# Performance work log

Hardware: AMD Instinct MI355X
Metric: run time of the kernel (lower is better)

## Reference

```python
import jax, jax.numpy as jnp
import numpy as np

EMBED_DIM = 1024
NUM_HEADS = 16
SCALE = (EMBED_DIM // NUM_HEADS) ** -0.5  # 0.125


def setup_inputs() -> dict:
    key = jax.random.key(0)
    ks = jax.random.split(key, 9)
    B, S, E = 4, 2048, EMBED_DIM
    std = E ** -0.5
    x = jax.random.normal(ks[0], (B, S, E), dtype=jnp.float32)
    Wq = jax.random.normal(ks[1], (E, E), dtype=jnp.float32) * std
    bq = jax.random.normal(ks[2], (E,), dtype=jnp.float32) * 0.01
    Wk = jax.random.normal(ks[3], (E, E), dtype=jnp.float32) * std
    bk = jax.random.normal(ks[4], (E,), dtype=jnp.float32) * 0.01
    Wv = jax.random.normal(ks[5], (E, E), dtype=jnp.float32) * std
    bv = jax.random.normal(ks[6], (E,), dtype=jnp.float32) * 0.01
    Wo = jax.random.normal(ks[7], (E, E), dtype=jnp.float32) * std
    bo = jax.random.normal(ks[8], (E,), dtype=jnp.float32) * 0.01
    return {"x": x, "Wq": Wq, "bq": bq, "Wk": Wk, "bk": bk,
            "Wv": Wv, "bv": bv, "Wo": Wo, "bo": bo}


def reference(x, Wq, bq, Wk, bk, Wv, bv, Wo, bo):
    # torch nn.Linear: y = x @ W.T + b
    q = jnp.einsum('bse,fe->bsf', x, Wq) + bq   # [B,S,E]
    k = jnp.einsum('bse,fe->bsf', x, Wk) + bk
    v = jnp.einsum('bse,fe->bsf', x, Wv) + bv
    # Bilinear (no softmax) attention: scores = (Q K^T) * scale
    scores = jnp.einsum('bse,bte->bst', q, k) * SCALE  # [B,S,S]
    out = jnp.einsum('bst,bte->bse', scores, v)        # [B,S,E]
    return jnp.einsum('bse,fe->bsf', out, Wo) + bo
```

## Files before the change

### kernel.cpp

```cpp
#include <hip/hip_runtime.h>
#include <stdint.h>

typedef __bf16 bf16_t;
typedef __bf16 bf16x8 __attribute__((ext_vector_type(8)));
typedef __bf16 bf16x4 __attribute__((ext_vector_type(4)));
typedef float floatx4 __attribute__((ext_vector_type(4)));

__device__ __forceinline__ void async_copy16(const bf16_t* g, bf16_t* l) {
  __builtin_amdgcn_global_load_lds(
      (const __attribute__((address_space(1))) void*)g,
      (__attribute__((address_space(3))) void*)l, 16, 0, 0);
}

struct CvtSeg { const float* s; bf16_t* d; long n; };
struct CvtArgs { CvtSeg seg[5]; };

__global__ void cvt_multi(CvtArgs a) {
  CvtSeg sg = a.seg[blockIdx.y];
#pragma unroll
  for (int it = 0; it < 4; it++) {
    long i = (((long)blockIdx.x + (long)it * 2048) * 256 + threadIdx.x) * 4;
    if (i < sg.n) {
      float4 f = *(const float4*)(sg.s + i);
      bf16x4 o;
      o[0] = (bf16_t)f.x; o[1] = (bf16_t)f.y; o[2] = (bf16_t)f.z; o[3] = (bf16_t)f.w;
      *(bf16x4*)(sg.d + i) = o;
    }
  }
}

__global__ __launch_bounds__(256, 2) void qkv3(
    const bf16_t* __restrict__ xb,
    const bf16_t* __restrict__ Wq, const bf16_t* __restrict__ Wk, const bf16_t* __restrict__ Wv,
    const float* __restrict__ bq, const float* __restrict__ bk, const float* __restrict__ bv,
    bf16_t* __restrict__ qout, bf16_t* __restrict__ kT, bf16_t* __restrict__ vT) {
  __shared__ bf16_t As[2 * 4096];
  __shared__ bf16_t Bsh[3][2 * 4096];
  const int L = blockIdx.x;
  const int V = (L & 7) * 64 + (L >> 3);
  const int batch = V >> 7;
  const int rr_   = V & 127;
  const int n0 = (rr_ & 7) * 128;
  const int m0 = (rr_ >> 3) * 128;

  const int tid = threadIdx.x, lane = tid & 63, w = tid >> 6;
  const int wr = w >> 1, wc = w & 1, quad = lane >> 4, lm = lane & 15;
  const int ar = lane >> 2;
  const int ak = (((lane & 3) ^ ((ar >> 1) & 3))) * 8;
  const int swz = (lm >> 1) & 3;

  const bf16_t* ag0 = xb + (long)batch * (2048L * 1024) + (long)(m0 + w * 16 + ar) * 1024 + ak;
  const bf16_t* ag1 = ag0 + 64L * 1024;
  const bf16_t* Wp[3] = {Wq, Wk, Wv};
  const bf16_t* bg0[3];
  const bf16_t* bg1[3];
#pragma unroll
  for (int p = 0; p < 3; p++) {
    bg0[p] = Wp[p] + (long)(n0 + w * 16 + ar) * 1024 + ak;
    bg1[p] = bg0[p] + 64L * 1024;
  }

  floatx4 acc[3][4][4];
#pragma unroll
  for (int p = 0; p < 3; p++)
#pragma unroll
    for (int r = 0; r < 4; r++)
#pragma unroll
      for (int c = 0; c < 4; c++)
        acc[p][r][c] = (floatx4){0.f, 0.f, 0.f, 0.f};

  {
    bf16_t* la = As + w * 512;
    async_copy16(ag0, la);
    async_copy16(ag1, la + 2048);
#pragma unroll
    for (int p = 0; p < 3; p++) {
      bf16_t* lb = Bsh[p] + w * 512;
      async_copy16(bg0[p], lb);
      async_copy16(bg1[p], lb + 2048);
    }
  }
  for (int i = 0; i < 32; i++) {
    __syncthreads();
    if (i + 1 < 32) {
      const int buf = (i + 1) & 1, k0 = (i + 1) * 32;
      bf16_t* la = As + buf * 4096 + w * 512;
      async_copy16(ag0 + k0, la);
      async_copy16(ag1 + k0, la + 2048);
#pragma unroll
      for (int p = 0; p < 3; p++) {
        bf16_t* lb = Bsh[p] + buf * 4096 + w * 512;
        async_copy16(bg0[p] + k0, lb);
        async_copy16(bg1[p] + k0, lb + 2048);
      }
    }
    const bf16_t* Ar = As + (i & 1) * 4096;
    bf16x8 afr[4];
#pragma unroll
    for (int r = 0; r < 4; r++)
      afr[r] = *(const bf16x8*)&Ar[(wr * 64 + r * 16 + lm) * 32 + (quad ^ swz) * 8];
#pragma unroll
    for (int p = 0; p < 3; p++) {
      const bf16_t* Br = Bsh[p] + (i & 1) * 4096;
      bf16x8 bfr[4];
#pragma unroll
      for (int c = 0; c < 4; c++)
        bfr[c] = *(const bf16x8*)&Br[(wc * 64 + c * 16 + lm) * 32 + (quad ^ swz) * 8];
#pragma unroll
      for (int r = 0; r < 4; r++)
#pragma unroll
        for (int c = 0; c < 4; c++)
          acc[p][r][c] = __builtin_amdgcn_mfma_f32_16x16x32_bf16(afr[r], bfr[c], acc[p][r][c], 0, 0, 0);
    }
  }

  const int rowBase = m0 + wr * 64, colBase = n0 + wc * 64;
  {
    bf16_t* C = qout + (long)batch * (2048L * 1024);
#pragma unroll
    for (int r = 0; r < 4; r++) {
      const int row = rowBase + r * 16 + quad * 4;
#pragma unroll
      for (int c = 0; c < 4; c++) {
        const int col = colBase + c * 16 + lm;
        const float bv_ = bq[col];
#pragma unroll
        for (int i = 0; i < 4; i++)
          C[(long)(row + i) * 1024 + col] = (bf16_t)(acc[0][r][c][i] + bv_);
      }
    }
  }
#pragma unroll
  for (int p = 1; p < 3; p++) {
    bf16_t* C = ((p == 1) ? kT : vT) + (long)batch * (1024L * 2048);
    const float* bias = (p == 1) ? bk : bv;
#pragma unroll
    for (int r = 0; r < 4; r++) {
      const int row = rowBase + r * 16 + quad * 4;
#pragma unroll
      for (int c = 0; c < 4; c++) {
        const int col = colBase + c * 16 + lm;
        const float bv_ = bias[col];
        bf16x4 pk;
#pragma unroll
        for (int i = 0; i < 4; i++) pk[i] = (bf16_t)(acc[p][r][c][i] + bv_);
        *(bf16x4*)(C + (long)col * 2048 + row) = pk;
      }
    }
  }
}

template<int OUT_MODE, bool HAS_BIAS, int TOTAL, int BPZ>
__global__ __launch_bounds__(256) void gemm_nt64(
    const bf16_t* __restrict__ A, const bf16_t* __restrict__ B,
    void* __restrict__ C, const float* __restrict__ bias,
    int lda, int ldb, int nk, long sA, long sB, long sC, int ldc, float alpha) {
  __shared__ bf16_t As[2 * 4096];
  __shared__ bf16_t Bs[2 * 2048];
  const int L = blockIdx.x;
  const int V = (L & 7) * (TOTAL / 8) + (L >> 3);
  const int batch = V / BPZ;
  const int r_ = V % BPZ;
  const int n0 = (r_ & 15) * 64;
  const int m0 = (r_ >> 4) * 128;

  const int tid = threadIdx.x, lane = tid & 63, w = tid >> 6;
  const int wr = w >> 1, wc = w & 1, quad = lane >> 4, lm = lane & 15;
  const int ar = lane >> 2;
  const int ak = (((lane & 3) ^ ((ar >> 1) & 3))) * 8;
  const int swz = (lm >> 1) & 3;

  const bf16_t* Ab = A + (long)batch * sA;
  const bf16_t* Bb = B + (long)batch * sB;
  const bf16_t* ag0 = Ab + (long)(m0 + w * 16 + ar) * lda + ak;
  const bf16_t* ag1 = ag0 + (long)64 * lda;
  const bf16_t* bg0 = Bb + (long)(n0 + w * 16 + ar) * ldb + ak;

  floatx4 acc[4][2];
#pragma unroll
  for (int r = 0; r < 4; r++)
#pragma unroll
    for (int c = 0; c < 2; c++) acc[r][c] = (floatx4){0.f, 0.f, 0.f, 0.f};

  {
    async_copy16(ag0, As + w * 512);
    async_copy16(ag1, As + w * 512 + 2048);
    async_copy16(bg0, Bs + w * 512);
  }
  for (int i = 0; i < nk; i++) {
    __syncthreads();
    if (i + 1 < nk) {
      const int buf = (i + 1) & 1, k0 = (i + 1) * 32;
      async_copy16(ag0 + k0, As + buf * 4096 + w * 512);
      async_copy16(ag1 + k0, As + buf * 4096 + w * 512 + 2048);
      async_copy16(bg0 + k0, Bs + buf * 2048 + w * 512);
    }
    const bf16_t* Ar = As + (i & 1) * 4096;
    const bf16_t* Br = Bs + (i & 1) * 2048;
    bf16x8 afr[4], bfr[2];
#pragma unroll
    for (int r = 0; r < 4; r++)
      afr[r] = *(const bf16x8*)&Ar[(wr * 64 + r * 16 + lm) * 32 + (quad ^ swz) * 8];
#pragma unroll
    for (int c = 0; c < 2; c++)
      bfr[c] = *(const bf16x8*)&Br[(wc * 32 + c * 16 + lm) * 32 + (quad ^ swz) * 8];
#pragma unroll
    for (int r = 0; r < 4; r++)
#pragma unroll
      for (int c = 0; c < 2; c++)
        acc[r][c] = __builtin_amdgcn_mfma_f32_16x16x32_bf16(afr[r], bfr[c], acc[r][c], 0, 0, 0);
  }

  const int rowBase = m0 + wr * 64, colBase = n0 + wc * 32;
  if (OUT_MODE == 0) {
    bf16_t* Cb = (bf16_t*)C + (long)batch * sC;
#pragma unroll
    for (int r = 0; r < 4; r++) {
      const int row = rowBase + r * 16 + quad * 4;
#pragma unroll
      for (int c = 0; c < 2; c++) {
        const int col = colBase + c * 16 + lm;
        const float bv_ = HAS_BIAS ? bias[col] : 0.f;
#pragma unroll
        for (int i = 0; i < 4; i++)
          Cb[(long)(row + i) * ldc + col] = (bf16_t)(acc[r][c][i] * alpha + bv_);
      }
    }
  } else {
    float* Cf = (float*)C + (long)batch * sC;
#pragma unroll
    for (int r = 0; r < 4; r++) {
      const int row = rowBase + r * 16 + quad * 4;
#pragma unroll
      for (int c = 0; c < 2; c++) {
        const int col = colBase + c * 16 + lm;
        const float bv_ = HAS_BIAS ? bias[col] : 0.f;
#pragma unroll
        for (int i = 0; i < 4; i++)
          Cf[(long)(row + i) * ldc + col] = acc[r][c][i] * alpha + bv_;
      }
    }
  }
}

extern "C" void kernel_launch(void* const* d_in, const int* in_sizes, int n_in,
                              void* d_out, int out_size, void* d_ws, size_t ws_size,
                              hipStream_t stream) {
  const float* x  = (const float*)d_in[0];
  const float* Wq = (const float*)d_in[1];
  const float* bq = (const float*)d_in[2];
  const float* Wk = (const float*)d_in[3];
  const float* bk = (const float*)d_in[4];
  const float* Wv = (const float*)d_in[5];
  const float* bv = (const float*)d_in[6];
  const float* Wo = (const float*)d_in[7];
  const float* bo = (const float*)d_in[8];
  float* out = (float*)d_out;

  const long NX = 8192L * 1024;
  const long NW = 1024L * 1024;
  const long NM = 4L * 1024 * 1024;

  bf16_t* ws  = (bf16_t*)d_ws;
  bf16_t* xb  = ws;
  bf16_t* Wqb = xb + NX;
  bf16_t* Wkb = Wqb + NW;
  bf16_t* Wvb = Wkb + NW;
  bf16_t* Wob = Wvb + NW;
  bf16_t* qb  = Wob + NW;
  bf16_t* kT  = qb + NX;
  bf16_t* vT  = kT + NX;
  bf16_t* MtTb = vT + NX;
  bf16_t* Gb   = xb;

  CvtArgs ca;
  ca.seg[0] = {x,  xb,  NX};
  ca.seg[1] = {Wq, Wqb, NW};
  ca.seg[2] = {Wk, Wkb, NW};
  ca.seg[3] = {Wv, Wvb, NW};
  ca.seg[4] = {Wo, Wob, NW};
  cvt_multi<<<dim3(2048, 5), 256, 0, stream>>>(ca);

  qkv3<<<dim3(512), 256, 0, stream>>>(xb, Wqb, Wkb, Wvb, bq, bk, bv, qb, kT, vT);

  gemm_nt64<0, false, 512, 128><<<dim3(512), 256, 0, stream>>>(
      kT, vT, MtTb, nullptr, 2048, 2048, 64,
      1024L * 2048, 1024L * 2048, 1024L * 1024, 1024, 0.125f);

  gemm_nt64<0, false, 512, 128><<<dim3(512), 256, 0, stream>>>(
      Wob, MtTb, Gb, nullptr, 1024, 1024, 32,
      0L, 1024L * 1024, 1024L * 1024, 1024, 1.0f);

  gemm_nt64<2, true, 1024, 256><<<dim3(1024), 256, 0, stream>>>(
      qb, Gb, out, bo, 1024, 1024, 32,
      2048L * 1024, 1024L * 1024, 2048L * 1024, 1024, 1.0f);
}
```

Baseline: 237.3 us.

## Use 128x128 tiles, split-K for K^T V, and reorder output GEMMs

```diff
diff --git a/kernel.cpp b/kernel.cpp
--- a/kernel.cpp
+++ b/kernel.cpp
@@ -27,6 +27,20 @@
       *(bf16x4*)(sg.d + i) = o;
     }
   }
+}
+
+__global__ void cvt_mhalf(const bf16_t* __restrict__ mh, bf16_t* __restrict__ mt) {
+  const long i = ((long)blockIdx.x * 256 + threadIdx.x) * 8;
+  const long b = i >> 20;
+  const long r = i & ((1L << 20) - 1);
+  const bf16_t* h0 = mh + ((b * 2) << 20) + r;
+  const bf16_t* h1 = h0 + (1L << 20);
+  bf16x8 x0 = *(const bf16x8*)h0;
+  bf16x8 x1 = *(const bf16x8*)h1;
+  bf16x8 o;
+#pragma unroll
+  for (int j = 0; j < 8; j++) o[j] = (bf16_t)((float)x0[j] + (float)x1[j]);
+  *(bf16x8*)(mt + i) = o;
 }
 
 __global__ __launch_bounds__(256, 2) void qkv3(
@@ -150,19 +164,21 @@
   }
 }
 
-template<int OUT_MODE, bool HAS_BIAS, int TOTAL, int BPZ>
-__global__ __launch_bounds__(256) void gemm_nt64(
+template<int OUT_MODE, bool HAS_BIAS, int TOTAL, int BPZ, int KSPLIT>
+__global__ __launch_bounds__(256) void gemm_nt128(
     const bf16_t* __restrict__ A, const bf16_t* __restrict__ B,
     void* __restrict__ C, const float* __restrict__ bias,
     int lda, int ldb, int nk, long sA, long sB, long sC, int ldc, float alpha) {
   __shared__ bf16_t As[2 * 4096];
-  __shared__ bf16_t Bs[2 * 2048];
+  __shared__ bf16_t Bs[2 * 4096];
   const int L = blockIdx.x;
   const int V = (L & 7) * (TOTAL / 8) + (L >> 3);
-  const int batch = V / BPZ;
+  const int zz = V / BPZ;
   const int r_ = V % BPZ;
-  const int n0 = (r_ & 15) * 64;
-  const int m0 = (r_ >> 4) * 128;
+  const int batch = zz / KSPLIT;
+  const long koff = (long)(zz % KSPLIT) * ((long)nk * 32);
+  const int n0 = (r_ & 7) * 128;
+  const int m0 = (r_ >> 3) * 128;
 
   const int tid = threadIdx.x, lane = tid & 63, w = tid >> 6;
   const int wr = w >> 1, wc = w & 1, quad = lane >> 4, lm = lane & 15;
@@ -170,22 +186,24 @@
   const int ak = (((lane & 3) ^ ((ar >> 1) & 3))) * 8;
   const int swz = (lm >> 1) & 3;
 
-  const bf16_t* Ab = A + (long)batch * sA;
-  const bf16_t* Bb = B + (long)batch * sB;
+  const bf16_t* Ab = A + (long)batch * sA + koff;
+  const bf16_t* Bb = B + (long)batch * sB + koff;
   const bf16_t* ag0 = Ab + (long)(m0 + w * 16 + ar) * lda + ak;
   const bf16_t* ag1 = ag0 + (long)64 * lda;
   const bf16_t* bg0 = Bb + (long)(n0 + w * 16 + ar) * ldb + ak;
-
-  floatx4 acc[4][2];
+  const bf16_t* bg1 = bg0 + (long)64 * ldb;
+
+  floatx4 acc[4][4];
 #pragma unroll
   for (int r = 0; r < 4; r++)
 #pragma unroll
-    for (int c = 0; c < 2; c++) acc[r][c] = (floatx4){0.f, 0.f, 0.f, 0.f};
+    for (int c = 0; c < 4; c++) acc[r][c] = (floatx4){0.f, 0.f, 0.f, 0.f};
 
   {
     async_copy16(ag0, As + w * 512);
     async_copy16(ag1, As + w * 512 + 2048);
     async_copy16(bg0, Bs + w * 512);
+    async_copy16(bg1, Bs + w * 512 + 2048);
   }
   for (int i = 0; i < nk; i++) {
     __syncthreads();
@@ -193,32 +211,33 @@
       const int buf = (i + 1) & 1, k0 = (i + 1) * 32;
       async_copy16(ag0 + k0, As + buf * 4096 + w * 512);
       async_copy16(ag1 + k0, As + buf * 4096 + w * 512 + 2048);
-      async_copy16(bg0 + k0, Bs + buf * 2048 + w * 512);
+      async_copy16(bg0 + k0, Bs + buf * 4096 + w * 512);
+      async_copy16(bg1 + k0, Bs + buf * 4096 + w * 512 + 2048);
     }
     const bf16_t* Ar = As + (i & 1) * 4096;
-    const bf16_t* Br = Bs + (i & 1) * 2048;
-    bf16x8 afr[4], bfr[2];
+    const bf16_t* Br = Bs + (i & 1) * 4096;
+    bf16x8 afr[4], bfr[4];
 #pragma unroll
     for (int r = 0; r < 4; r++)
       afr[r] = *(const bf16x8*)&Ar[(wr * 64 + r * 16 + lm) * 32 + (quad ^ swz) * 8];
 #pragma unroll
-    for (int c = 0; c < 2; c++)
-      bfr[c] = *(const bf16x8*)&Br[(wc * 32 + c * 16 + lm) * 32 + (quad ^ swz) * 8];
+    for (int c = 0; c < 4; c++)
+      bfr[c] = *(const bf16x8*)&Br[(wc * 64 + c * 16 + lm) * 32 + (quad ^ swz) * 8];
 #pragma unroll
     for (int r = 0; r < 4; r++)
 #pragma unroll
-      for (int c = 0; c < 2; c++)
+      for (int c = 0; c < 4; c++)
         acc[r][c] = __builtin_amdgcn_mfma_f32_16x16x32_bf16(afr[r], bfr[c], acc[r][c], 0, 0, 0);
   }
 
-  const int rowBase = m0 + wr * 64, colBase = n0 + wc * 32;
+  const int rowBase = m0 + wr * 64, colBase = n0 + wc * 64;
   if (OUT_MODE == 0) {
-    bf16_t* Cb = (bf16_t*)C + (long)batch * sC;
+    bf16_t* Cb = (bf16_t*)C + (long)zz * sC;
 #pragma unroll
     for (int r = 0; r < 4; r++) {
       const int row = rowBase + r * 16 + quad * 4;
 #pragma unroll
-      for (int c = 0; c < 2; c++) {
+      for (int c = 0; c < 4; c++) {
         const int col = colBase + c * 16 + lm;
         const float bv_ = HAS_BIAS ? bias[col] : 0.f;
 #pragma unroll
@@ -227,12 +246,12 @@
       }
     }
   } else {
-    float* Cf = (float*)C + (long)batch * sC;
+    float* Cf = (float*)C + (long)zz * sC;
 #pragma unroll
     for (int r = 0; r < 4; r++) {
       const int row = rowBase + r * 16 + quad * 4;
 #pragma unroll
-      for (int c = 0; c < 2; c++) {
+      for (int c = 0; c < 4; c++) {
         const int col = colBase + c * 16 + lm;
         const float bv_ = HAS_BIAS ? bias[col] : 0.f;
 #pragma unroll
@@ -259,7 +278,6 @@
 
   const long NX = 8192L * 1024;
   const long NW = 1024L * 1024;
-  const long NM = 4L * 1024 * 1024;
 
   bf16_t* ws  = (bf16_t*)d_ws;
   bf16_t* xb  = ws;
@@ -270,8 +288,9 @@
   bf16_t* qb  = Wob + NW;
   bf16_t* kT  = qb + NX;
   bf16_t* vT  = kT + NX;
-  bf16_t* MtTb = vT + NX;
-  bf16_t* Gb   = xb;
+  bf16_t* Mh  = xb;
+  bf16_t* Mtb = kT;
+  bf16_t* Pb  = vT;
 
   CvtArgs ca;
   ca.seg[0] = {x,  xb,  NX};
@@ -283,15 +302,17 @@
 
   qkv3<<<dim3(512), 256, 0, stream>>>(xb, Wqb, Wkb, Wvb, bq, bk, bv, qb, kT, vT);
 
-  gemm_nt64<0, false, 512, 128><<<dim3(512), 256, 0, stream>>>(
-      kT, vT, MtTb, nullptr, 2048, 2048, 64,
+  gemm_nt128<0, false, 512, 64, 2><<<dim3(512), 256, 0, stream>>>(
+      vT, kT, Mh, nullptr, 2048, 2048, 32,
       1024L * 2048, 1024L * 2048, 1024L * 1024, 1024, 0.125f);
 
-  gemm_nt64<0, false, 512, 128><<<dim3(512), 256, 0, stream>>>(
-      Wob, MtTb, Gb, nullptr, 1024, 1024, 32,
-      0L, 1024L * 1024, 1024L * 1024, 1024, 1.0f);
-
-  gemm_nt64<2, true, 1024, 256><<<dim3(1024), 256, 0, stream>>>(
-      qb, Gb, out, bo, 1024, 1024, 32,
+  cvt_mhalf<<<dim3(2048), 256, 0, stream>>>(Mh, Mtb);
+
+  gemm_nt128<0, false, 512, 128, 1><<<dim3(512), 256, 0, stream>>>(
+      qb, Mtb, Pb, nullptr, 1024, 1024, 32,
       2048L * 1024, 1024L * 1024, 2048L * 1024, 1024, 1.0f);
-}
+
+  gemm_nt128<2, true, 512, 128, 1><<<dim3(512), 256, 0, stream>>>(
+      Pb, Wob, out, bo, 1024, 1024, 32,
+      2048L * 1024, 0L, 2048L * 1024, 1024, 1.0f);
+}
```

Result: no change. 239.5 us (+0.9%).

## Use per-warp private LDS staging with 128x128 tiles in GEMMs

Applied to the files above, without the earlier changes.

```diff
diff --git a/kernel.cpp b/kernel.cpp
--- a/kernel.cpp
+++ b/kernel.cpp
@@ -151,18 +151,17 @@
 }
 
 template<int OUT_MODE, bool HAS_BIAS, int TOTAL, int BPZ>
-__global__ __launch_bounds__(256) void gemm_nt64(
+__global__ __launch_bounds__(256) void gemm_wp(
     const bf16_t* __restrict__ A, const bf16_t* __restrict__ B,
     void* __restrict__ C, const float* __restrict__ bias,
     int lda, int ldb, int nk, long sA, long sB, long sC, int ldc, float alpha) {
-  __shared__ bf16_t As[2 * 4096];
-  __shared__ bf16_t Bs[2 * 2048];
+  __shared__ bf16_t Ls[4 * 8192];
   const int L = blockIdx.x;
   const int V = (L & 7) * (TOTAL / 8) + (L >> 3);
   const int batch = V / BPZ;
   const int r_ = V % BPZ;
-  const int n0 = (r_ & 15) * 64;
-  const int m0 = (r_ >> 4) * 128;
+  const int n0 = (r_ & 7) * 128;
+  const int m0 = (r_ >> 3) * 128;
 
   const int tid = threadIdx.x, lane = tid & 63, w = tid >> 6;
   const int wr = w >> 1, wc = w & 1, quad = lane >> 4, lm = lane & 15;
@@ -170,55 +169,61 @@
   const int ak = (((lane & 3) ^ ((ar >> 1) & 3))) * 8;
   const int swz = (lm >> 1) & 3;
 
+  bf16_t* Lw = Ls + w * 8192;
   const bf16_t* Ab = A + (long)batch * sA;
   const bf16_t* Bb = B + (long)batch * sB;
-  const bf16_t* ag0 = Ab + (long)(m0 + w * 16 + ar) * lda + ak;
-  const bf16_t* ag1 = ag0 + (long)64 * lda;
-  const bf16_t* bg0 = Bb + (long)(n0 + w * 16 + ar) * ldb + ak;
-
-  floatx4 acc[4][2];
+  const bf16_t* agA = Ab + (long)(m0 + wr * 64 + ar) * lda + ak;
+  const bf16_t* agB = Bb + (long)(n0 + wc * 64 + ar) * ldb + ak;
+
+  auto STAGE = [&](int t, int b) {
+    const int k0 = t * 32;
+    bf16_t* d = Lw + b * 4096;
+#pragma unroll
+    for (int j = 0; j < 4; j++)
+      async_copy16(agA + (long)j * 16 * lda + k0, d + j * 512);
+#pragma unroll
+    for (int j = 0; j < 4; j++)
+      async_copy16(agB + (long)j * 16 * ldb + k0, d + 2048 + j * 512);
+  };
+
+  floatx4 acc[4][4];
 #pragma unroll
   for (int r = 0; r < 4; r++)
 #pragma unroll
-    for (int c = 0; c < 2; c++) acc[r][c] = (floatx4){0.f, 0.f, 0.f, 0.f};
-
-  {
-    async_copy16(ag0, As + w * 512);
-    async_copy16(ag1, As + w * 512 + 2048);
-    async_copy16(bg0, Bs + w * 512);
-  }
+    for (int c = 0; c < 4; c++) acc[r][c] = (floatx4){0.f, 0.f, 0.f, 0.f};
+
+  STAGE(0, 0);
   for (int i = 0; i < nk; i++) {
-    __syncthreads();
     if (i + 1 < nk) {
-      const int buf = (i + 1) & 1, k0 = (i + 1) * 32;
-      async_copy16(ag0 + k0, As + buf * 4096 + w * 512);
-      async_copy16(ag1 + k0, As + buf * 4096 + w * 512 + 2048);
-      async_copy16(bg0 + k0, Bs + buf * 2048 + w * 512);
-    }
-    const bf16_t* Ar = As + (i & 1) * 4096;
-    const bf16_t* Br = Bs + (i & 1) * 2048;
-    bf16x8 afr[4], bfr[2];
+      STAGE(i + 1, (i + 1) & 1);
+      asm volatile("s_waitcnt vmcnt(8)" ::: "memory");
+    } else {
+      asm volatile("s_waitcnt vmcnt(0)" ::: "memory");
+    }
+    const bf16_t* Aw = Lw + (i & 1) * 4096;
+    const bf16_t* Bw = Aw + 2048;
+    bf16x8 afr[4], bfr[4];
 #pragma unroll
     for (int r = 0; r < 4; r++)
-      afr[r] = *(const bf16x8*)&Ar[(wr * 64 + r * 16 + lm) * 32 + (quad ^ swz) * 8];
-#pragma unroll
-    for (int c = 0; c < 2; c++)
-      bfr[c] = *(const bf16x8*)&Br[(wc * 32 + c * 16 + lm) * 32 + (quad ^ swz) * 8];
+      afr[r] = *(const bf16x8*)&Aw[(r * 16 + lm) * 32 + (quad ^ swz) * 8];
+#pragma unroll
+    for (int c = 0; c < 4; c++)
+      bfr[c] = *(const bf16x8*)&Bw[(c * 16 + lm) * 32 + (quad ^ swz) * 8];
 #pragma unroll
     for (int r = 0; r < 4; r++)
 #pragma unroll
-      for (int c = 0; c < 2; c++)
+      for (int c = 0; c < 4; c++)
         acc[r][c] = __builtin_amdgcn_mfma_f32_16x16x32_bf16(afr[r], bfr[c], acc[r][c], 0, 0, 0);
   }
 
-  const int rowBase = m0 + wr * 64, colBase = n0 + wc * 32;
+  const int rowBase = m0 + wr * 64, colBase = n0 + wc * 64;
   if (OUT_MODE == 0) {
     bf16_t* Cb = (bf16_t*)C + (long)batch * sC;
 #pragma unroll
     for (int r = 0; r < 4; r++) {
       const int row = rowBase + r * 16 + quad * 4;
 #pragma unroll
-      for (int c = 0; c < 2; c++) {
+      for (int c = 0; c < 4; c++) {
         const int col = colBase + c * 16 + lm;
         const float bv_ = HAS_BIAS ? bias[col] : 0.f;
 #pragma unroll
@@ -232,7 +237,7 @@
     for (int r = 0; r < 4; r++) {
       const int row = rowBase + r * 16 + quad * 4;
 #pragma unroll
-      for (int c = 0; c < 2; c++) {
+      for (int c = 0; c < 4; c++) {
         const int col = colBase + c * 16 + lm;
         const float bv_ = HAS_BIAS ? bias[col] : 0.f;
 #pragma unroll
@@ -259,7 +264,6 @@
 
   const long NX = 8192L * 1024;
   const long NW = 1024L * 1024;
-  const long NM = 4L * 1024 * 1024;
 
   bf16_t* ws  = (bf16_t*)d_ws;
   bf16_t* xb  = ws;
@@ -270,8 +274,8 @@
   bf16_t* qb  = Wob + NW;
   bf16_t* kT  = qb + NX;
   bf16_t* vT  = kT + NX;
-  bf16_t* MtTb = vT + NX;
-  bf16_t* Gb   = xb;
+  bf16_t* MtTb = xb;
+  bf16_t* Gb   = vT;
 
   CvtArgs ca;
   ca.seg[0] = {x,  xb,  NX};
@@ -283,15 +287,15 @@
 
   qkv3<<<dim3(512), 256, 0, stream>>>(xb, Wqb, Wkb, Wvb, bq, bk, bv, qb, kT, vT);
 
-  gemm_nt64<0, false, 512, 128><<<dim3(512), 256, 0, stream>>>(
+  gemm_wp<0, false, 256, 64><<<dim3(256), 256, 0, stream>>>(
       kT, vT, MtTb, nullptr, 2048, 2048, 64,
       1024L * 2048, 1024L * 2048, 1024L * 1024, 1024, 0.125f);
 
-  gemm_nt64<0, false, 512, 128><<<dim3(512), 256, 0, stream>>>(
+  gemm_wp<0, false, 256, 64><<<dim3(256), 256, 0, stream>>>(
       Wob, MtTb, Gb, nullptr, 1024, 1024, 32,
       0L, 1024L * 1024, 1024L * 1024, 1024, 1.0f);
 
-  gemm_nt64<2, true, 1024, 256><<<dim3(1024), 256, 0, stream>>>(
+  gemm_wp<2, true, 512, 128><<<dim3(512), 256, 0, stream>>>(
       qb, Gb, out, bo, 1024, 1024, 32,
       2048L * 1024, 1024L * 1024, 2048L * 1024, 1024, 1.0f);
 }
```

Measured after the change: 231.7 us. -2.4%, faster.
